# Kernel optimization log

Hardware: AMD Instinct MI355X
Metric: run time of the kernel (lower is better)

Reference implementation:

```python
import jax, jax.numpy as jnp
import numpy as np

KS = 3          # kernel size
PAD = 1         # padding
N = KS * KS     # number of sampling taps (9)


def setup_inputs() -> dict:
    key = jax.random.key(0)
    k0, k1, k2 = jax.random.split(key, 3)
    B, Cin, Cout, H, W = 4, 64, 64, 128, 128
    x = jax.random.normal(k0, (B, Cin, H, W), jnp.float32)
    # offset conv is zero-initialized in the original; use small random weights
    # so the sampling pattern is actually irregular (post-training behavior)
    w_off = jax.random.normal(k1, (2 * N, Cin, KS, KS), jnp.float32) * 0.05
    b_off = jnp.zeros((2 * N,), jnp.float32)
    w_def = jax.random.normal(k2, (Cout, Cin, KS, KS), jnp.float32) / np.float32(np.sqrt(Cin * N))
    b_def = jnp.zeros((Cout,), jnp.float32)
    return {"x": x, "w_off": w_off, "b_off": b_off, "w_def": w_def, "b_def": b_def}


def _conv3x3(x, w, b):
    y = jax.lax.conv_general_dilated(
        x, w, window_strides=(1, 1), padding=((PAD, PAD), (PAD, PAD)),
        dimension_numbers=("NCHW", "OIHW", "NCHW"))
    return y + b[None, :, None, None]


def _deform_forward(x, w_off, b_off, w_def, b_def):
    B, C, H, W = x.shape
    Cout = w_def.shape[0]
    offset = _conv3x3(x, w_off, b_off)                 # [B, 2N, H, W]

    xp = jnp.pad(x, ((0, 0), (0, 0), (PAD, PAD), (PAD, PAD)))  # zero pad
    Hp, Wp = H + 2 * PAD, W + 2 * PAD

    # sampling positions p = p0 + pn + offset (coords in padded frame)
    r = jnp.arange(-(KS // 2), KS // 2 + 1, dtype=x.dtype)
    pn_x = jnp.repeat(r, KS)          # [-1,-1,-1, 0,0,0, 1,1,1]
    pn_y = jnp.tile(r, KS)            # [-1, 0, 1, ...]
    p0x = jnp.arange(1, H + 1, dtype=x.dtype)[None, :, None, None]  # [1,H,1,1]
    p0y = jnp.arange(1, W + 1, dtype=x.dtype)[None, None, :, None]  # [1,1,W,1]
    offx = offset[:, :N].transpose(0, 2, 3, 1)          # [B,H,W,N]
    offy = offset[:, N:].transpose(0, 2, 3, 1)
    px = p0x + pn_x[None, None, None, :] + offx          # [B,H,W,N]
    py = p0y + pn_y[None, None, None, :] + offy

    # integer corners (floor has zero grad == detach in torch ref)
    flx, fly = jnp.floor(px), jnp.floor(py)
    qlx = jnp.clip(flx, 0, Hp - 1)
    qly = jnp.clip(fly, 0, Wp - 1)
    qrx = jnp.clip(flx + 1, 0, Hp - 1)
    qry = jnp.clip(fly + 1, 0, Wp - 1)
    pxc = jnp.clip(px, 0, Hp - 1)
    pyc = jnp.clip(py, 0, Wp - 1)

    # bilinear weights (matches torch DeformConv2D formulas)
    g_lt = (1 + (qlx - pxc)) * (1 + (qly - pyc))
    g_rb = (1 - (qrx - pxc)) * (1 - (qry - pyc))
    g_lb = (1 + (qlx - pxc)) * (1 - (qry - pyc))
    g_rt = (1 - (qrx - pxc)) * (1 + (qly - pyc))

    xf = xp.reshape(B, C, Hp * Wp)

    def gather(xfb, ix, iy):
        idx = (ix * Wp + iy).astype(jnp.int32).reshape(-1)
        return xfb[:, idx].reshape(C, H, W, N)

    g4 = jax.vmap(gather)
    x_lt = g4(xf, qlx, qly)   # [B,C,H,W,N]
    x_rb = g4(xf, qrx, qry)
    x_lb = g4(xf, qlx, qry)
    x_rt = g4(xf, qrx, qly)

    x_off = (g_lt[:, None] * x_lt + g_rb[:, None] * x_rb
             + g_lb[:, None] * x_lb + g_rt[:, None] * x_rt)  # [B,C,H,W,N]

    out = jnp.einsum("bchwn,ocn->bohw", x_off, w_def.reshape(Cout, C, N))
    return out + b_def[None, :, None, None]


def reference(x, w_off, b_off, w_def, b_def):
    return _deform_forward(x, w_off, b_off, w_def, b_def)
```

## Files before the change

kernel.cpp:

```cpp
#include <hip/hip_runtime.h>

#define B_   4
#define CIN  64
#define COUT 64
#define H_   128
#define W_   128
#define NOFF 18
#define HW   (H_ * W_)
#define HP   130
#define WP   130

typedef __attribute__((ext_vector_type(8))) short bf16x8;
typedef __attribute__((ext_vector_type(4))) float f32x4;

__device__ __forceinline__ unsigned short f2bf(float f) {
    unsigned int u = __float_as_uint(f);
    return (unsigned short)((u + 0x7fffu + ((u >> 16) & 1u)) >> 16);
}
__device__ __forceinline__ float bf2f(unsigned short s) {
    return __uint_as_float(((unsigned int)s) << 16);
}

__global__ __launch_bounds__(256) void k_wt(
    const float* __restrict__ w_def, const float* __restrict__ w_off,
    unsigned short* __restrict__ wB, unsigned short* __restrict__ wBo)
{
    const int i = blockIdx.x * 256 + threadIdx.x;
    if (i < 18 * 4 * 64) {
        const int kblk = i >> 8;
        const int nblk = (i >> 6) & 3;
        const int lane = i & 63;
        const int o = nblk * 16 + (lane & 15);
        unsigned int pk[4];
#pragma unroll
        for (int d = 0; d < 4; ++d) {
            unsigned int v = 0;
#pragma unroll
            for (int e = 0; e < 2; ++e) {
                const int K = kblk * 32 + 8 * (lane >> 4) + d * 2 + e;
                const int n = K >> 6, c = K & 63;
                v |= (unsigned int)f2bf(w_def[((size_t)o * 64 + c) * 9 + n]) << (16 * e);
            }
            pk[d] = v;
        }
        *(uint4*)(wB + (size_t)i * 8) = make_uint4(pk[0], pk[1], pk[2], pk[3]);
    }
    const int j = i - 18 * 4 * 64;
    if (j >= 0 && j < 18 * 2 * 64) {
        const int kblk = j >> 7;
        const int nblk = (j >> 6) & 1;
        const int lane = j & 63;
        const int o = nblk * 16 + (lane & 15);
        unsigned int pk[4];
#pragma unroll
        for (int d = 0; d < 4; ++d) {
            unsigned int v = 0;
#pragma unroll
            for (int e = 0; e < 2; ++e) {
                const int K = kblk * 32 + 8 * (lane >> 4) + d * 2 + e;
                const int n = K >> 6, c = K & 63;
                const float wv = (o < NOFF) ? w_off[((size_t)o * 64 + c) * 9 + n] : 0.f;
                v |= (unsigned int)f2bf(wv) << (16 * e);
            }
            pk[d] = v;
        }
        *(uint4*)(wBo + (size_t)j * 8) = make_uint4(pk[0], pk[1], pk[2], pk[3]);
    }
}

__global__ __launch_bounds__(256) void k_xt(
    const float* __restrict__ x, unsigned short* __restrict__ xt)
{
    const int b  = blockIdx.x / HP;
    const int hp = blockIdx.x - b * HP;
    const int c  = threadIdx.x & 63;
    const int wq = threadIdx.x >> 6;
    unsigned short* dst = xt + (((size_t)b * HP + hp) * WP) * 64 + c;
    for (int wp = wq; wp < WP; wp += 4) {
        float v = 0.f;
        if (hp >= 1 && hp <= H_ && wp >= 1 && wp <= W_)
            v = x[(((size_t)b * CIN + c) * H_ + (hp - 1)) * W_ + (wp - 1)];
        dst[(size_t)wp * 64] = f2bf(v);
    }
}

__global__ __launch_bounds__(256) void k_offconv_mfma(
    const unsigned short* __restrict__ xt, const unsigned short* __restrict__ wBo,
    const float* __restrict__ b_off, float* __restrict__ off)
{
    const int tid  = threadIdx.x;
    const int lane = tid & 63;
    const int wv   = tid >> 6;
    const int row  = lane & 15;
    const int g    = lane >> 4;

    const int p0 = blockIdx.x * 64 + wv * 16;
    const int b  = p0 >> 14;
    const int h  = (p0 >> 7) & 127;
    const int w0 = p0 & 127;

    const unsigned short* xtb = xt + (size_t)b * (HP * WP * 64);
    const unsigned short* Bp  = wBo + (size_t)lane * 8;

    f32x4 acc0 = {0.f, 0.f, 0.f, 0.f};
    f32x4 acc1 = {0.f, 0.f, 0.f, 0.f};

#pragma unroll
    for (int kb = 0; kb < 18; ++kb) {
        const int n  = kb >> 1;
        const int hp = h + n / 3;
        const int wp = w0 + row + (n % 3);
        const int cb = (kb & 1) * 32 + g * 8;
        const bf16x8 a  = *(const bf16x8*)(xtb + ((size_t)hp * WP + wp) * 64 + cb);
        const bf16x8 b0 = *(const bf16x8*)(Bp + (size_t)(kb * 2 + 0) * 512);
        const bf16x8 b1 = *(const bf16x8*)(Bp + (size_t)(kb * 2 + 1) * 512);
        acc0 = __builtin_amdgcn_mfma_f32_16x16x32_bf16(a, b0, acc0, 0, 0, 0);
        acc1 = __builtin_amdgcn_mfma_f32_16x16x32_bf16(a, b1, acc1, 0, 0, 0);
    }

    const int hwb = (p0 + 4 * g) & 16383;
    {
        const int o = row;
        float4 v = make_float4(acc0[0] + b_off[o], acc0[1] + b_off[o],
                               acc0[2] + b_off[o], acc0[3] + b_off[o]);
        *(float4*)&off[((size_t)b * NOFF + o) * HW + hwb] = v;
    }
    if (row < 2) {
        const int o = 16 + row;
        float4 v = make_float4(acc1[0] + b_off[o], acc1[1] + b_off[o],
                               acc1[2] + b_off[o], acc1[3] + b_off[o]);
        *(float4*)&off[((size_t)b * NOFF + o) * HW + hwb] = v;
    }
}

__global__ __launch_bounds__(256) void k_fuse(
    const unsigned short* __restrict__ xt, const float* __restrict__ off,
    unsigned short* __restrict__ xoff, const unsigned short* __restrict__ wB,
    const float* __restrict__ b_def, float* __restrict__ out)
{
    const int tid   = threadIdx.x;
    const int lane  = tid & 63;
    const int wv    = tid >> 6;
    const int pxblk = blockIdx.x;
    const int b     = pxblk >> 9;
    const int h     = (pxblk >> 2) & 127;
    const int w0    = (pxblk & 3) * 32;

    __shared__ uint4  geoI[9][32];
    __shared__ float4 geoG[9][32];

    if (lane < 32) {
        const int wpix = w0 + lane;
        const float* offp = off + ((size_t)b * NOFF) * HW + h * W_ + wpix;
        for (int n = wv; n < 9; n += 4) {
            const float ox = offp[(size_t)n * HW];
            const float oy = offp[(size_t)(n + 9) * HW];
            const float px = (float)(h + n / 3) + ox;
            const float py = (float)(wpix + n % 3) + oy;
            const float flx = floorf(px), fly = floorf(py);
            const float qlx = fminf(fmaxf(flx, 0.f), 129.f);
            const float qly = fminf(fmaxf(fly, 0.f), 129.f);
            const float qrx = fminf(fmaxf(flx + 1.f, 0.f), 129.f);
            const float qry = fminf(fmaxf(fly + 1.f, 0.f), 129.f);
            const float pxc = fminf(fmaxf(px, 0.f), 129.f);
            const float pyc = fminf(fmaxf(py, 0.f), 129.f);
            const float gxl = 1.f + (qlx - pxc);
            const float gxr = 1.f - (qrx - pxc);
            const float gyl = 1.f + (qly - pyc);
            const float gyr = 1.f - (qry - pyc);
            const int xl = (int)qlx, yl = (int)qly, xr = (int)qrx, yr = (int)qry;
            geoI[n][lane] = make_uint4((unsigned)((xl * WP + yl) * 128),
                                       (unsigned)((xr * WP + yr) * 128),
                                       (unsigned)((xl * WP + yr) * 128),
                                       (unsigned)((xr * WP + yl) * 128));
            geoG[n][lane] = make_float4(gxl * gyl, gxr * gyr, gxl * gyr, gxr * gyl);
        }
    }
    __syncthreads();

    const char* xtb2 = (const char*)(xt + (size_t)b * (HP * WP * 64)) + lane * 2;
    unsigned short* xo = xoff + (size_t)(pxblk * 32) * 576;

#pragma unroll 1
    for (int pxi = 0; pxi < 8; ++pxi) {
        const int pxl = wv * 8 + pxi;
#pragma unroll 3
        for (int n = 0; n < 9; ++n) {
            const uint4  gi = geoI[n][pxl];
            const float4 gg = geoG[n][pxl];
            const float vlt = bf2f(*(const unsigned short*)(xtb2 + gi.x));
            const float vrb = bf2f(*(const unsigned short*)(xtb2 + gi.y));
            const float vlb = bf2f(*(const unsigned short*)(xtb2 + gi.z));
            const float vrt = bf2f(*(const unsigned short*)(xtb2 + gi.w));
            const float v = fmaf(gg.x, vlt, fmaf(gg.y, vrb,
                            fmaf(gg.z, vlb, gg.w * vrt)));
            xo[(size_t)pxl * 576 + n * 64 + lane] = f2bf(v);
        }
    }

    __syncthreads();
    if (wv >= 2) return;

    const int row = lane & 15;
    const int g   = lane >> 4;

    const unsigned short* Ap = xoff + (size_t)(pxblk * 32 + wv * 16 + row) * 576 + g * 8;
    const unsigned short* Bp = wB + (size_t)lane * 8;

    f32x4 acc0 = {0.f, 0.f, 0.f, 0.f};
    f32x4 acc1 = {0.f, 0.f, 0.f, 0.f};
    f32x4 acc2 = {0.f, 0.f, 0.f, 0.f};
    f32x4 acc3 = {0.f, 0.f, 0.f, 0.f};

#pragma unroll 3
    for (int kb = 0; kb < 18; ++kb) {
        const bf16x8 a  = *(const bf16x8*)(Ap + kb * 32);
        const bf16x8 b0 = *(const bf16x8*)(Bp + (size_t)(kb * 4 + 0) * 512);
        const bf16x8 b1 = *(const bf16x8*)(Bp + (size_t)(kb * 4 + 1) * 512);
        const bf16x8 b2 = *(const bf16x8*)(Bp + (size_t)(kb * 4 + 2) * 512);
        const bf16x8 b3 = *(const bf16x8*)(Bp + (size_t)(kb * 4 + 3) * 512);
        acc0 = __builtin_amdgcn_mfma_f32_16x16x32_bf16(a, b0, acc0, 0, 0, 0);
        acc1 = __builtin_amdgcn_mfma_f32_16x16x32_bf16(a, b1, acc1, 0, 0, 0);
        acc2 = __builtin_amdgcn_mfma_f32_16x16x32_bf16(a, b2, acc2, 0, 0, 0);
        acc3 = __builtin_amdgcn_mfma_f32_16x16x32_bf16(a, b3, acc3, 0, 0, 0);
    }

    const int p_base = pxblk * 32 + wv * 16 + 4 * g;
#pragma unroll
    for (int i = 0; i < 4; ++i) {
        const int o = i * 16 + row;
        const float bias = b_def[o];
        const f32x4 A = (i == 0) ? acc0 : (i == 1) ? acc1 : (i == 2) ? acc2 : acc3;
#pragma unroll
        for (int r = 0; r < 4; ++r) {
            const int p  = p_base + r;
            const int bb = p >> 14;
            const int hw = p & 16383;
            out[((size_t)(bb * COUT + o)) * HW + hw] = A[r] + bias;
        }
    }
}

extern "C" void kernel_launch(void* const* d_in, const int* in_sizes, int n_in,
                              void* d_out, int out_size, void* d_ws, size_t ws_size,
                              hipStream_t stream)
{
    const float* x     = (const float*)d_in[0];
    const float* w_off = (const float*)d_in[1];
    const float* b_off = (const float*)d_in[2];
    const float* w_def = (const float*)d_in[3];
    const float* b_def = (const float*)d_in[4];
    float* out = (float*)d_out;

    char* ws = (char*)d_ws;
    float*          off  = (float*)(ws + 0);
    unsigned short* wB   = (unsigned short*)(ws + 4718592);
    unsigned short* wBo  = (unsigned short*)(ws + 4792320);
    unsigned short* xt   = (unsigned short*)(ws + 4829184);
    unsigned short* xoff = (unsigned short*)(ws + 13481984);

    k_wt<<<(18 * 4 * 64 + 18 * 2 * 64 + 255) / 256, 256, 0, stream>>>(
        w_def, w_off, wB, wBo);
    k_xt<<<B_ * HP, 256, 0, stream>>>(x, xt);
    k_offconv_mfma<<<B_ * HW / 64, 256, 0, stream>>>(xt, wBo, b_off, off);
    k_fuse<<<B_ * HW / 32, 256, 0, stream>>>(xt, off, xoff, wB, b_def, out);
}
```

Before: 86.18 us.

## Pack horizontally adjacent pixels into paired layout to halve bilinear gathers

```diff
diff --git a/kernel.cpp b/kernel.cpp
--- a/kernel.cpp
+++ b/kernel.cpp
@@ -16,9 +16,6 @@
 __device__ __forceinline__ unsigned short f2bf(float f) {
     unsigned int u = __float_as_uint(f);
     return (unsigned short)((u + 0x7fffu + ((u >> 16) & 1u)) >> 16);
-}
-__device__ __forceinline__ float bf2f(unsigned short s) {
-    return __uint_as_float(((unsigned int)s) << 16);
 }
 
 __global__ __launch_bounds__(256) void k_wt(
@@ -84,6 +81,22 @@
     }
 }
 
+__global__ __launch_bounds__(256) void k_xt2(
+    const unsigned short* __restrict__ xt, unsigned int* __restrict__ xt2)
+{
+    const int b  = blockIdx.x / HP;
+    const int hp = blockIdx.x - b * HP;
+    const int c  = threadIdx.x & 63;
+    const int wq = threadIdx.x >> 6;
+    const unsigned short* src = xt + (((size_t)b * HP + hp) * WP) * 64 + c;
+    unsigned int* dst = xt2 + (((size_t)b * HP + hp) * WP) * 64 + c;
+    for (int wp = wq; wp < WP; wp += 4) {
+        unsigned int lo = src[(size_t)wp * 64];
+        unsigned int hi = (wp + 1 < WP) ? (unsigned int)src[(size_t)(wp + 1) * 64] : 0u;
+        dst[(size_t)wp * 64] = lo | (hi << 16);
+    }
+}
+
 __global__ __launch_bounds__(256) void k_offconv_mfma(
     const unsigned short* __restrict__ xt, const unsigned short* __restrict__ wBo,
     const float* __restrict__ b_off, float* __restrict__ off)
@@ -94,7 +107,9 @@
     const int row  = lane & 15;
     const int g    = lane >> 4;
 
-    const int p0 = blockIdx.x * 64 + wv * 16;
+    const int lb = ((blockIdx.x & 7) << 7) | (blockIdx.x >> 3);
+
+    const int p0 = lb * 64 + wv * 16;
     const int b  = p0 >> 14;
     const int h  = (p0 >> 7) & 127;
     const int w0 = p0 & 127;
@@ -134,19 +149,19 @@
 }
 
 __global__ __launch_bounds__(256) void k_fuse(
-    const unsigned short* __restrict__ xt, const float* __restrict__ off,
+    const unsigned int* __restrict__ xt2, const float* __restrict__ off,
     unsigned short* __restrict__ xoff, const unsigned short* __restrict__ wB,
     const float* __restrict__ b_def, float* __restrict__ out)
 {
     const int tid   = threadIdx.x;
     const int lane  = tid & 63;
     const int wv    = tid >> 6;
-    const int pxblk = blockIdx.x;
+    const int pxblk = ((blockIdx.x & 7) << 8) | (blockIdx.x >> 3);
     const int b     = pxblk >> 9;
     const int h     = (pxblk >> 2) & 127;
     const int w0    = (pxblk & 3) * 32;
 
-    __shared__ uint4  geoI[9][32];
+    __shared__ uint2  geoI[9][32];
     __shared__ float4 geoG[9][32];
 
     if (lane < 32) {
@@ -169,16 +184,16 @@
             const float gyl = 1.f + (qly - pyc);
             const float gyr = 1.f - (qry - pyc);
             const int xl = (int)qlx, yl = (int)qly, xr = (int)qrx, yr = (int)qry;
-            geoI[n][lane] = make_uint4((unsigned)((xl * WP + yl) * 128),
-                                       (unsigned)((xr * WP + yr) * 128),
-                                       (unsigned)((xl * WP + yr) * 128),
-                                       (unsigned)((xr * WP + yl) * 128));
-            geoG[n][lane] = make_float4(gxl * gyl, gxr * gyr, gxl * gyr, gxr * gyl);
+            float wyl = gyl, wyr = gyr;
+            if (yr == yl) { wyl = gyl + gyr; wyr = 0.f; }
+            geoI[n][lane] = make_uint2((unsigned)((xl * WP + yl) * 256),
+                                       (unsigned)((xr * WP + yl) * 256));
+            geoG[n][lane] = make_float4(wyl, wyr, gxl, gxr);
         }
     }
     __syncthreads();
 
-    const char* xtb2 = (const char*)(xt + (size_t)b * (HP * WP * 64)) + lane * 2;
+    const char* xtb4 = (const char*)(xt2 + (size_t)b * (HP * WP * 64)) + lane * 4;
     unsigned short* xo = xoff + (size_t)(pxblk * 32) * 576;
 
 #pragma unroll 1
@@ -186,14 +201,17 @@
         const int pxl = wv * 8 + pxi;
 #pragma unroll 3
         for (int n = 0; n < 9; ++n) {
-            const uint4  gi = geoI[n][pxl];
+            const uint2  gi = geoI[n][pxl];
             const float4 gg = geoG[n][pxl];
-            const float vlt = bf2f(*(const unsigned short*)(xtb2 + gi.x));
-            const float vrb = bf2f(*(const unsigned short*)(xtb2 + gi.y));
-            const float vlb = bf2f(*(const unsigned short*)(xtb2 + gi.z));
-            const float vrt = bf2f(*(const unsigned short*)(xtb2 + gi.w));
-            const float v = fmaf(gg.x, vlt, fmaf(gg.y, vrb,
-                            fmaf(gg.z, vlb, gg.w * vrt)));
+            const unsigned int u1 = *(const unsigned int*)(xtb4 + gi.x);
+            const unsigned int u2 = *(const unsigned int*)(xtb4 + gi.y);
+            const float s0 = __uint_as_float(u1 << 16);
+            const float s1 = __uint_as_float(u1 & 0xffff0000u);
+            const float t0 = __uint_as_float(u2 << 16);
+            const float t1 = __uint_as_float(u2 & 0xffff0000u);
+            const float r1 = fmaf(gg.x, s0, gg.y * s1);
+            const float r2 = fmaf(gg.x, t0, gg.y * t1);
+            const float v  = fmaf(gg.z, r1, gg.w * r2);
             xo[(size_t)pxl * 576 + n * 64 + lane] = f2bf(v);
         }
     }
@@ -257,11 +275,13 @@
     unsigned short* wB   = (unsigned short*)(ws + 4718592);
     unsigned short* wBo  = (unsigned short*)(ws + 4792320);
     unsigned short* xt   = (unsigned short*)(ws + 4829184);
-    unsigned short* xoff = (unsigned short*)(ws + 13481984);
+    unsigned int*   xt2  = (unsigned int*)(ws + 13481984);
+    unsigned short* xoff = (unsigned short*)(ws + 30787584);
 
     k_wt<<<(18 * 4 * 64 + 18 * 2 * 64 + 255) / 256, 256, 0, stream>>>(
         w_def, w_off, wB, wBo);
     k_xt<<<B_ * HP, 256, 0, stream>>>(x, xt);
+    k_xt2<<<B_ * HP, 256, 0, stream>>>(xt, xt2);
     k_offconv_mfma<<<B_ * HW / 64, 256, 0, stream>>>(xt, wBo, b_off, off);
-    k_fuse<<<B_ * HW / 32, 256, 0, stream>>>(xt, off, xoff, wB, b_def, out);
-}
+    k_fuse<<<B_ * HW / 32, 256, 0, stream>>>(xt2, off, xoff, wB, b_def, out);
+}
```

Result: slower. 94.26 us (+9.4%).
